# Kernel optimization log

Hardware: AMD Instinct MI355X
Metric: run time of the kernel (lower is better)

## Reference

```python
import jax, jax.numpy as jnp
import numpy as np

PADDING_INDEX = -1


def setup_inputs() -> dict:
    key = jax.random.key(0)
    B, S, T = 32, 512, 64
    log_potentials = jax.random.normal(key, (B, S, T, T), dtype=jnp.float32)
    mask = jnp.ones((B, S), dtype=bool)
    return {"log_potentials": log_potentials, "mask": mask}


def _viterbi(log_potentials):
    # log_potentials: [B, S, T, T]; entry [b, s, i, j] = score of transitioning
    # from tag i at step s-1 to tag j at step s (initial prev tag is free).
    P = jnp.transpose(log_potentials, (1, 0, 2, 3))  # [S, B, T, T]

    # Step 0: maximize over the free initial previous tag.
    alpha0 = jnp.max(P[0], axis=1)  # [B, T]

    def step(alpha, p):
        # max-plus recurrence: scores[b, i, j] = alpha[b, i] + p[b, i, j]
        scores = alpha[:, :, None] + p          # [B, T, T]
        bp = jnp.argmax(scores, axis=1)          # [B, T] best prev tag
        return jnp.max(scores, axis=1), bp

    alpha_last, bps = jax.lax.scan(step, alpha0, P[1:])  # bps: [S-1, B, T]
    last_tag = jnp.argmax(alpha_last, axis=-1)           # [B]

    def back(tag, bp):
        prev = jnp.take_along_axis(bp, tag[:, None], axis=1)[:, 0]  # [B]
        return prev, prev

    # Backtrace from step S-1 down to step 0.
    _, prev_tags = jax.lax.scan(back, last_tag, bps, reverse=True)  # [S-1, B]
    tags = jnp.concatenate([prev_tags, last_tag[None]], axis=0)     # [S, B]
    return tags.T  # [B, S]


def reference(log_potentials, mask):
    tags = _viterbi(log_potentials)
    # padded positions get padding_index (matches tags*mask + pad*~mask)
    return jnp.where(mask, tags, PADDING_INDEX)
```

## Files before the change

### kernel.cpp

```cpp
#include <hip/hip_runtime.h>

namespace {

constexpr int T = 64;
constexpr int S = 512;
constexpr int B = 32;
constexpr int DEPTH = 6;

#define WAIT_VM20() asm volatile("s_waitcnt vmcnt(20)" ::: "memory")
#define WAIT_VM0()  asm volatile("s_waitcnt vmcnt(0)" ::: "memory")
#define WAIT_LGKM() asm volatile("s_waitcnt lgkmcnt(0)" ::: "memory")
#define CBAR()      asm volatile("" ::: "memory")

__device__ __forceinline__ void load16(const float* g, float* l) {
  __builtin_amdgcn_global_load_lds(
      (const __attribute__((address_space(1))) void*)g,
      (__attribute__((address_space(3))) void*)l, 16, 0, 0);
}

__device__ __forceinline__ unsigned int f2s(float f) {
  unsigned int u = __float_as_uint(f);
  return u ^ (unsigned int)(((int)u >> 31) | 0x80000000);
}
__device__ __forceinline__ float s2f(unsigned int u) {
  u ^= (u & 0x80000000u) ? 0x80000000u : 0xFFFFFFFFu;
  return __uint_as_float(u);
}

__global__ __launch_bounds__(256, 1) void viterbi_fwd(
    const float* __restrict__ P,
    const int* __restrict__ mask,
    int* __restrict__ out)
{
  __shared__ __align__(16) float lds_p[DEPTH * T * T];
  __shared__ __align__(16) float lds_alpha[2][T];
  __shared__ __align__(16) unsigned long long lds_part[4][T];
  __shared__ __align__(16) unsigned char lds_bp[S * T];

  const int tid = threadIdx.x;
  const int j   = tid & 63;
  const int w   = tid >> 6;
  const int b   = blockIdx.x;
  const float* Pb = P + (size_t)b * S * T * T;

  if (tid < T) lds_alpha[0][tid] = 0.0f;

  for (int d = 0; d < DEPTH; ++d) {
    const float* gs = Pb + d * (T * T) + w * 1024 + j * 4;
    float* ls = &lds_p[d * (T * T) + w * 1024];
#pragma unroll
    for (int r = 0; r < 4; ++r) load16(gs + r * 256, ls + r * 256);
  }
  WAIT_LGKM(); __builtin_amdgcn_s_barrier(); CBAR();

  float last_alpha = 0.0f;
  int slot = 0;
  int next_src = DEPTH;

  for (int s = 0; s < S; ++s) {
    WAIT_VM20();

    float a[16];
    {
      const float4* ap = (const float4*)&lds_alpha[s & 1][w * 16];
#pragma unroll
      for (int r = 0; r < 4; ++r) {
        float4 v = ap[r];
        a[4 * r + 0] = v.x; a[4 * r + 1] = v.y;
        a[4 * r + 2] = v.z; a[4 * r + 3] = v.w;
      }
    }

    const float* pb = &lds_p[slot * (T * T) + w * 1024 + j];
    float best = a[0] + pb[0];
    int bi = w * 16;
#pragma unroll
    for (int k = 1; k < 16; ++k) {
      float sc = a[k] + pb[k * 64];
      bool g = sc > best;
      bi   = g ? (w * 16 + k) : bi;
      best = g ? sc : best;
    }

    lds_part[w][j] = ((unsigned long long)f2s(best) << 32) | (unsigned int)(255 - bi);
    WAIT_LGKM(); __builtin_amdgcn_s_barrier(); CBAR();

    unsigned long long m = lds_part[0][j];
#pragma unroll
    for (int q = 1; q < 4; ++q) {
      unsigned long long t2 = lds_part[q][j];
      m = (t2 > m) ? t2 : m;
    }
    last_alpha = s2f((unsigned int)(m >> 32));
    const int bnew = 255 - (int)(m & 0xFFu);
    if (w == 0) {
      lds_alpha[(s + 1) & 1][j] = last_alpha;
      lds_bp[s * 64 + j] = (unsigned char)bnew;
    }
    WAIT_LGKM(); __builtin_amdgcn_s_barrier(); CBAR();

    {
      int src = next_src; if (src >= S) src -= S;
      const float* gs = Pb + src * (T * T) + w * 1024 + j * 4;
      float* ls = &lds_p[slot * (T * T) + w * 1024];
#pragma unroll
      for (int r = 0; r < 4; ++r) load16(gs + r * 256, ls + r * 256);
      ++next_src;
    }
    ++slot; if (slot == DEPTH) slot = 0;
  }

  if (w == 0) {
    unsigned long long mm =
        ((unsigned long long)f2s(last_alpha) << 32) | (unsigned int)(63 - j);
#pragma unroll
    for (int off = 32; off >= 1; off >>= 1) {
      unsigned int hi = (unsigned int)(mm >> 32), lo = (unsigned int)mm;
      unsigned int ohi = __shfl_xor(hi, off, 64);
      unsigned int olo = __shfl_xor(lo, off, 64);
      unsigned long long o = ((unsigned long long)ohi << 32) | olo;
      mm = (o > mm) ? o : mm;
    }
    const int last_tag = 63 - (int)(mm & 0xFFu);
    if (tid == 0) {
      const int* mrow = mask + b * S;
      int* orow = out + b * S;
      int tag = last_tag;
      orow[S - 1] = mrow[S - 1] ? tag : -1;
      for (int s = S - 1; s >= 1; --s) {
        tag = lds_bp[s * 64 + tag];
        orow[s - 1] = mrow[s - 1] ? tag : -1;
      }
    }
  }
  WAIT_VM0();
}

}

extern "C" void kernel_launch(void* const* d_in, const int* in_sizes, int n_in,
                              void* d_out, int out_size, void* d_ws, size_t ws_size,
                              hipStream_t stream) {
  const float* P = (const float*)d_in[0];
  const int* mask = (const int*)d_in[1];
  int* out = (int*)d_out;
  (void)in_sizes; (void)n_in; (void)out_size; (void)d_ws; (void)ws_size;
  hipLaunchKernelGGL(viterbi_fwd, dim3(B), dim3(256), 0, stream, P, mask, out);
}
```

Measured before the change: 889.3 us.

## Run Viterbi recurrence in a single wavefront with shuffle reductions

```diff
diff --git a/kernel.cpp b/kernel.cpp
--- a/kernel.cpp
+++ b/kernel.cpp
@@ -5,12 +5,11 @@
 constexpr int T = 64;
 constexpr int S = 512;
 constexpr int B = 32;
-constexpr int DEPTH = 6;
+constexpr int DEPTH = 4;
 
-#define WAIT_VM20() asm volatile("s_waitcnt vmcnt(20)" ::: "memory")
+#define WAIT_VM48() asm volatile("s_waitcnt vmcnt(48)" ::: "memory")
 #define WAIT_VM0()  asm volatile("s_waitcnt vmcnt(0)" ::: "memory")
 #define WAIT_LGKM() asm volatile("s_waitcnt lgkmcnt(0)" ::: "memory")
-#define CBAR()      asm volatile("" ::: "memory")
 
 __device__ __forceinline__ void load16(const float* g, float* l) {
   __builtin_amdgcn_global_load_lds(
@@ -20,119 +19,127 @@
 
 __device__ __forceinline__ unsigned int f2s(float f) {
   unsigned int u = __float_as_uint(f);
-  return u ^ (unsigned int)(((int)u >> 31) | 0x80000000);
+  return u ^ (unsigned int)(((int)u >> 31) | 0x80000000u);
 }
 __device__ __forceinline__ float s2f(unsigned int u) {
   u ^= (u & 0x80000000u) ? 0x80000000u : 0xFFFFFFFFu;
   return __uint_as_float(u);
 }
 
-__global__ __launch_bounds__(256, 1) void viterbi_fwd(
+__device__ __forceinline__ unsigned long long u64max_x(unsigned long long v, int xm) {
+  unsigned int hi = __shfl_xor((unsigned int)(v >> 32), xm, 64);
+  unsigned int lo = __shfl_xor((unsigned int)(v & 0xFFFFFFFFu), xm, 64);
+  unsigned long long o = ((unsigned long long)hi << 32) | lo;
+  return (o > v) ? o : v;
+}
+
+__global__ __launch_bounds__(64, 1) void viterbi_1w(
     const float* __restrict__ P,
     const int* __restrict__ mask,
     int* __restrict__ out)
 {
-  __shared__ __align__(16) float lds_p[DEPTH * T * T];
-  __shared__ __align__(16) float lds_alpha[2][T];
-  __shared__ __align__(16) unsigned long long lds_part[4][T];
-  __shared__ __align__(16) unsigned char lds_bp[S * T];
+  __shared__ __align__(16) float ring[DEPTH * T * T];
+  __shared__ __align__(16) float alpha[2][T];
+  __shared__ __align__(16) unsigned char bp[S * T];
+  __shared__ __align__(16) int tag_seq[S];
 
-  const int tid = threadIdx.x;
-  const int j   = tid & 63;
-  const int w   = tid >> 6;
-  const int b   = blockIdx.x;
+  const int l  = threadIdx.x;
+  const int c4 = l & 15;
+  const int r4 = l >> 4;
+  const int b  = blockIdx.x;
   const float* Pb = P + (size_t)b * S * T * T;
 
-  if (tid < T) lds_alpha[0][tid] = 0.0f;
+  if (r4 == 0) *(float4*)&alpha[0][c4 * 4] = float4{0.f, 0.f, 0.f, 0.f};
 
   for (int d = 0; d < DEPTH; ++d) {
-    const float* gs = Pb + d * (T * T) + w * 1024 + j * 4;
-    float* ls = &lds_p[d * (T * T) + w * 1024];
 #pragma unroll
-    for (int r = 0; r < 4; ++r) load16(gs + r * 256, ls + r * 256);
+    for (int m = 0; m < 16; ++m)
+      load16(Pb + d * 4096 + m * 256 + l * 4, &ring[d * 4096 + m * 256]);
   }
-  WAIT_LGKM(); __builtin_amdgcn_s_barrier(); CBAR();
-
-  float last_alpha = 0.0f;
-  int slot = 0;
-  int next_src = DEPTH;
+  WAIT_LGKM();
 
   for (int s = 0; s < S; ++s) {
-    WAIT_VM20();
+    WAIT_VM48();
+    const float* base = &ring[(s & 3) * 4096 + r4 * 1024 + c4 * 4];
 
     float a[16];
-    {
-      const float4* ap = (const float4*)&lds_alpha[s & 1][w * 16];
 #pragma unroll
-      for (int r = 0; r < 4; ++r) {
-        float4 v = ap[r];
-        a[4 * r + 0] = v.x; a[4 * r + 1] = v.y;
-        a[4 * r + 2] = v.z; a[4 * r + 3] = v.w;
-      }
+    for (int q = 0; q < 4; ++q) {
+      float4 v = *(const float4*)&alpha[s & 1][r4 * 16 + q * 4];
+      a[4*q] = v.x; a[4*q+1] = v.y; a[4*q+2] = v.z; a[4*q+3] = v.w;
     }
 
-    const float* pb = &lds_p[slot * (T * T) + w * 1024 + j];
-    float best = a[0] + pb[0];
-    int bi = w * 16;
+    float best0, best1, best2, best3;
+    int bi0 = 0, bi1 = 0, bi2 = 0, bi3 = 0;
+    {
+      float4 p0 = *(const float4*)(base);
+      best0 = a[0] + p0.x; best1 = a[0] + p0.y;
+      best2 = a[0] + p0.z; best3 = a[0] + p0.w;
+    }
 #pragma unroll
     for (int k = 1; k < 16; ++k) {
-      float sc = a[k] + pb[k * 64];
-      bool g = sc > best;
-      bi   = g ? (w * 16 + k) : bi;
-      best = g ? sc : best;
+      float4 pk_ = *(const float4*)(base + k * 64);
+      float s0 = a[k] + pk_.x; if (s0 > best0) { best0 = s0; bi0 = k; }
+      float s1 = a[k] + pk_.y; if (s1 > best1) { best1 = s1; bi1 = k; }
+      float s2 = a[k] + pk_.z; if (s2 > best2) { best2 = s2; bi2 = k; }
+      float s3 = a[k] + pk_.w; if (s3 > best3) { best3 = s3; bi3 = k; }
     }
 
-    lds_part[w][j] = ((unsigned long long)f2s(best) << 32) | (unsigned int)(255 - bi);
-    WAIT_LGKM(); __builtin_amdgcn_s_barrier(); CBAR();
+    const int rbase = r4 * 16;
+    unsigned long long k0 = ((unsigned long long)f2s(best0) << 32) | (unsigned)(255 - (rbase + bi0));
+    unsigned long long k1 = ((unsigned long long)f2s(best1) << 32) | (unsigned)(255 - (rbase + bi1));
+    unsigned long long k2 = ((unsigned long long)f2s(best2) << 32) | (unsigned)(255 - (rbase + bi2));
+    unsigned long long k3 = ((unsigned long long)f2s(best3) << 32) | (unsigned)(255 - (rbase + bi3));
+    k0 = u64max_x(k0, 16); k0 = u64max_x(k0, 32);
+    k1 = u64max_x(k1, 16); k1 = u64max_x(k1, 32);
+    k2 = u64max_x(k2, 16); k2 = u64max_x(k2, 32);
+    k3 = u64max_x(k3, 16); k3 = u64max_x(k3, 32);
 
-    unsigned long long m = lds_part[0][j];
+    const int bn0 = 255 - (int)(k0 & 0xFF), bn1 = 255 - (int)(k1 & 0xFF);
+    const int bn2 = 255 - (int)(k2 & 0xFF), bn3 = 255 - (int)(k3 & 0xFF);
+    if (r4 == 0) {
+      *(unsigned int*)&bp[s * 64 + c4 * 4] =
+          (unsigned)bn0 | ((unsigned)bn1 << 8) | ((unsigned)bn2 << 16) | ((unsigned)bn3 << 24);
+      *(float4*)&alpha[(s + 1) & 1][c4 * 4] =
+          float4{s2f((unsigned)(k0 >> 32)), s2f((unsigned)(k1 >> 32)),
+                 s2f((unsigned)(k2 >> 32)), s2f((unsigned)(k3 >> 32))};
+    }
+    WAIT_LGKM();
+
+    int src = s + DEPTH; if (src >= S) src -= S;
 #pragma unroll
-    for (int q = 1; q < 4; ++q) {
-      unsigned long long t2 = lds_part[q][j];
-      m = (t2 > m) ? t2 : m;
-    }
-    last_alpha = s2f((unsigned int)(m >> 32));
-    const int bnew = 255 - (int)(m & 0xFFu);
-    if (w == 0) {
-      lds_alpha[(s + 1) & 1][j] = last_alpha;
-      lds_bp[s * 64 + j] = (unsigned char)bnew;
-    }
-    WAIT_LGKM(); __builtin_amdgcn_s_barrier(); CBAR();
-
-    {
-      int src = next_src; if (src >= S) src -= S;
-      const float* gs = Pb + src * (T * T) + w * 1024 + j * 4;
-      float* ls = &lds_p[slot * (T * T) + w * 1024];
-#pragma unroll
-      for (int r = 0; r < 4; ++r) load16(gs + r * 256, ls + r * 256);
-      ++next_src;
-    }
-    ++slot; if (slot == DEPTH) slot = 0;
+    for (int m = 0; m < 16; ++m)
+      load16(Pb + src * 4096 + m * 256 + l * 4, &ring[(s & 3) * 4096 + m * 256]);
   }
 
-  if (w == 0) {
-    unsigned long long mm =
-        ((unsigned long long)f2s(last_alpha) << 32) | (unsigned int)(63 - j);
-#pragma unroll
-    for (int off = 32; off >= 1; off >>= 1) {
-      unsigned int hi = (unsigned int)(mm >> 32), lo = (unsigned int)mm;
-      unsigned int ohi = __shfl_xor(hi, off, 64);
-      unsigned int olo = __shfl_xor(lo, off, 64);
-      unsigned long long o = ((unsigned long long)ohi << 32) | olo;
-      mm = (o > mm) ? o : mm;
-    }
-    const int last_tag = 63 - (int)(mm & 0xFFu);
-    if (tid == 0) {
-      const int* mrow = mask + b * S;
-      int* orow = out + b * S;
-      int tag = last_tag;
-      orow[S - 1] = mrow[S - 1] ? tag : -1;
-      for (int s = S - 1; s >= 1; --s) {
-        tag = lds_bp[s * 64 + tag];
-        orow[s - 1] = mrow[s - 1] ? tag : -1;
-      }
+  float4 fa = *(const float4*)&alpha[0][c4 * 4];
+  unsigned long long mm = ((unsigned long long)f2s(fa.x) << 32) | (unsigned)(63 - (4 * c4 + 0));
+  unsigned long long tt;
+  tt = ((unsigned long long)f2s(fa.y) << 32) | (unsigned)(63 - (4 * c4 + 1)); if (tt > mm) mm = tt;
+  tt = ((unsigned long long)f2s(fa.z) << 32) | (unsigned)(63 - (4 * c4 + 2)); if (tt > mm) mm = tt;
+  tt = ((unsigned long long)f2s(fa.w) << 32) | (unsigned)(63 - (4 * c4 + 3)); if (tt > mm) mm = tt;
+  mm = u64max_x(mm, 1); mm = u64max_x(mm, 2); mm = u64max_x(mm, 4);
+  mm = u64max_x(mm, 8); mm = u64max_x(mm, 16); mm = u64max_x(mm, 32);
+  const int last_tag = 63 - (int)(mm & 0xFF);
+
+  if (l == 0) {
+    int tag = last_tag;
+    tag_seq[S - 1] = tag;
+    for (int s = S - 1; s >= 1; --s) {
+      tag = bp[s * 64 + tag];
+      tag_seq[s - 1] = tag;
     }
   }
+  WAIT_LGKM();
+
+  const int* mrow = mask + b * S;
+  int* orow = out + b * S;
+#pragma unroll
+  for (int q = 0; q < S / 64; ++q) {
+    int s2 = l + q * 64;
+    orow[s2] = mrow[s2] ? tag_seq[s2] : -1;
+  }
+
   WAIT_VM0();
 }
 
@@ -145,5 +152,5 @@
   const int* mask = (const int*)d_in[1];
   int* out = (int*)d_out;
   (void)in_sizes; (void)n_in; (void)out_size; (void)d_ws; (void)ws_size;
-  hipLaunchKernelGGL(viterbi_fwd, dim3(B), dim3(256), 0, stream, P, mask, out);
+  hipLaunchKernelGGL(viterbi_1w, dim3(B), dim3(64), 0, stream, P, mask, out);
 }
```

Result: slower. 1.084 ms (+21.9%).
